# Performance work log

Measured on AMD Instinct MI355X. Metric: run time of the kernel, lower is better.

Reference implementation:

```python
import jax, jax.numpy as jnp
import numpy as np
from jax import lax


def _dense_image_warp(img, flow):
    # TFA semantics: out[b,i,j] = bilinear_sample(img[b], (i - flow[b,i,j,0], j - flow[b,i,j,1]))
    # floors clamped to [0, size-2]; alphas clamped to [0, 1].
    B, H, W, C = img.shape
    gy = jnp.arange(H, dtype=flow.dtype)[None, :, None]
    gx = jnp.arange(W, dtype=flow.dtype)[None, None, :]
    qy = gy - flow[..., 0]
    qx = gx - flow[..., 1]
    fy = jnp.clip(jnp.floor(qy), 0.0, H - 2)
    fx = jnp.clip(jnp.floor(qx), 0.0, W - 2)
    ay = jnp.clip(qy - fy, 0.0, 1.0)[..., None]
    ax = jnp.clip(qx - fx, 0.0, 1.0)[..., None]
    fy = fy.astype(jnp.int32)
    fx = fx.astype(jnp.int32)
    b = jnp.arange(B)[:, None, None]
    tl = img[b, fy, fx]
    tr = img[b, fy, fx + 1]
    bl = img[b, fy + 1, fx]
    br = img[b, fy + 1, fx + 1]
    top = tl + ax * (tr - tl)
    bot = bl + ax * (br - bl)
    return top + ay * (bot - top)


def _conv(x, w, b, act):
    y = lax.conv_general_dilated(x, w, (1, 1), 'SAME',
                                 dimension_numbers=('NHWC', 'HWIO', 'NHWC')) + b
    return jax.nn.relu(y) if act else y


def _predict(x, ws, bs):
    for i in range(4):
        x = _conv(x, ws[i], bs[i], True)
    return _conv(x, ws[4], bs[4], False)  # final 1x1 -> 2 channels, linear


def _upsample2x(x):
    B, H, W, C = x.shape
    return jax.image.resize(x, (B, 2 * H, 2 * W, C), method='bilinear')


# Conv stack dims: in=64 (concat of two 32-ch maps)
_KSHAPES = [(3, 3, 64, 32), (3, 3, 32, 64), (1, 1, 64, 64), (1, 1, 64, 16), (1, 1, 16, 2)]


def setup_inputs() -> dict:
    key = jax.random.key(0)
    ks = jax.random.split(key, 4 + 2 * len(_KSHAPES))
    B, H, W, C = 8, 256, 256, 32
    inp = {
        'input_1': jax.random.normal(ks[0], (B, H, W, C), jnp.float32),
        'input_2': jax.random.normal(ks[1], (B, H, W, C), jnp.float32),
        'flow_1_2': jax.random.normal(ks[2], (B, H, W, 2), jnp.float32) * 3.0,
        'flow_2_1': jax.random.normal(ks[3], (B, H, W, 2), jnp.float32) * 3.0,
    }
    for i, sh in enumerate(_KSHAPES):
        inp[f'w12_{i}'] = jax.random.normal(ks[4 + i], sh, jnp.float32) * 0.05
        inp[f'b12_{i}'] = jnp.zeros((sh[-1],), jnp.float32)
        inp[f'w21_{i}'] = jax.random.normal(ks[4 + len(_KSHAPES) + i], sh, jnp.float32) * 0.05
        inp[f'b21_{i}'] = jnp.zeros((sh[-1],), jnp.float32)
    return inp


def reference(input_1, input_2, flow_1_2, flow_2_1,
              w12_0, b12_0, w12_1, b12_1, w12_2, b12_2, w12_3, b12_3, w12_4, b12_4,
              w21_0, b21_0, w21_1, b21_1, w21_2, b21_2, w21_3, b21_3, w21_4, b21_4):
    ws12 = [w12_0, w12_1, w12_2, w12_3, w12_4]
    bs12 = [b12_0, b12_1, b12_2, b12_3, b12_4]
    ws21 = [w21_0, w21_1, w21_2, w21_3, w21_4]
    bs21 = [b21_0, b21_1, b21_2, b21_3, b21_4]

    # 1 -> 2 direction
    input_1_warped_1 = _dense_image_warp(input_1, flow_1_2)
    flow_change_1_2 = _predict(jnp.concatenate([input_2, input_1_warped_1], axis=3), ws12, bs12)
    flow_1_2_changed = flow_1_2 + flow_change_1_2
    input_1_warped_2 = _dense_image_warp(input_1, flow_1_2_changed)
    flow_1_2_up = _upsample2x(flow_1_2_changed)

    # 2 -> 1 direction
    input_2_warped_1 = _dense_image_warp(input_2, flow_2_1)
    flow_change_2_1 = _predict(jnp.concatenate([input_1, input_2_warped_1], axis=3), ws21, bs21)
    flow_2_1_changed = flow_2_1 + flow_change_2_1
    input_2_warped_2 = _dense_image_warp(input_2, flow_2_1_changed)
    flow_2_1_up = _upsample2x(flow_2_1_changed)

    return (input_1_warped_2, input_2_warped_2, flow_1_2_up, flow_2_1_up)
```

## Files before the change

kernel.cpp:

```cpp
#include <hip/hip_runtime.h>
#include <hip/hip_bf16.h>
#include <cstddef>

#define B_ 8
#define H_ 256
#define W_ 256

static constexpr int NPIX = B_ * H_ * W_;

typedef __attribute__((ext_vector_type(8))) short bf16x8;
typedef __attribute__((ext_vector_type(4))) float f32x4;

__device__ __forceinline__ float4 ld4(const float* p) { return *(const float4*)p; }

__device__ __forceinline__ short f2bf(float x) {
    unsigned u = __float_as_uint(x);
    unsigned r = (u + 0x7fffu + ((u >> 16) & 1u)) >> 16;
    return (short)r;
}

__global__ __launch_bounds__(256) void cvt_inputs_kernel(
    const float* __restrict__ in1, const float* __restrict__ in2,
    short* __restrict__ xb1, short* __restrict__ xb2)
{
    int t = blockIdx.x * 256 + threadIdx.x;
    const int N8 = NPIX * 32 / 8;
    const float* src = (t < N8) ? in1 : in2;
    short* dst = (t < N8) ? xb1 : xb2;
    int i = (t < N8) ? t : t - N8;
    float4 a = ld4(src + (size_t)i * 8);
    float4 b = ld4(src + (size_t)i * 8 + 4);
    bf16x8 r;
    r[0] = f2bf(a.x); r[1] = f2bf(a.y); r[2] = f2bf(a.z); r[3] = f2bf(a.w);
    r[4] = f2bf(b.x); r[5] = f2bf(b.y); r[6] = f2bf(b.z); r[7] = f2bf(b.w);
    *(bf16x8*)(dst + (size_t)i * 8) = r;
}

__global__ __launch_bounds__(256) void prep_weights_kernel(
    const float* __restrict__ w0a, const float* __restrict__ w1a,
    const float* __restrict__ w2a, const float* __restrict__ w3a,
    const float* __restrict__ w0b, const float* __restrict__ w1b,
    const float* __restrict__ w2b, const float* __restrict__ w3b,
    short* __restrict__ wt0, short* __restrict__ wt1)
{
    int t = blockIdx.x * 256 + threadIdx.x;
    if (t >= 2 * 5248) return;
    int dir = t / 5248;
    int r = t % 5248;
    const float* w0 = dir ? w0b : w0a;
    const float* w1 = dir ? w1b : w1a;
    const float* w2 = dir ? w2b : w2a;
    const float* w3 = dir ? w3b : w3a;
    short* wt = dir ? wt1 : wt0;
    bf16x8 v;
    if (r < 2304) {
        int l = r & 63, n = (r >> 6) & 1, c = (r >> 7) & 1, tp = r >> 8;
#pragma unroll
        for (int j = 0; j < 8; ++j) {
            int ci = c * 32 + 8 * (l >> 4) + j;
            int co = n * 16 + (l & 15);
            v[j] = f2bf(w0[(size_t)(tp * 64 + ci) * 32 + co]);
        }
    } else if (r < 4608) {
        int q = r - 2304;
        int l = q & 63, n = (q >> 6) & 3, tp = q >> 8;
#pragma unroll
        for (int j = 0; j < 8; ++j) {
            int ci = 8 * (l >> 4) + j;
            int co = n * 16 + (l & 15);
            v[j] = f2bf(w1[(size_t)(tp * 32 + ci) * 64 + co]);
        }
    } else if (r < 5120) {
        int q = r - 4608;
        int l = q & 63, n = (q >> 6) & 3, c = q >> 8;
#pragma unroll
        for (int j = 0; j < 8; ++j) {
            int k = 32 * c + 8 * (l >> 4) + j;
            int co = n * 16 + (l & 15);
            v[j] = f2bf(w2[(size_t)k * 64 + co]);
        }
    } else {
        int q = r - 5120;
        int l = q & 63, c = q >> 6;
#pragma unroll
        for (int j = 0; j < 8; ++j) {
            int k = 32 * c + 8 * (l >> 4) + j;
            v[j] = f2bf(w3[(size_t)k * 16 + (l & 15)]);
        }
    }
    *(bf16x8*)(wt + (size_t)r * 8) = v;
}

__global__ __launch_bounds__(256) void warp_bf16_kernel(
    const float* __restrict__ img, const float* __restrict__ flow,
    short* __restrict__ out)
{
    int gid = blockIdx.x * 256 + threadIdx.x;
    int p   = gid >> 3;
    int c4  = (gid & 7) << 2;
    int b   = p >> 16;
    int i   = (p >> 8) & 255;
    int j   = p & 255;
    float2 f = *(const float2*)(flow + (size_t)p * 2);
    float qy = (float)i - f.x;
    float qx = (float)j - f.y;
    float fyf = fminf(fmaxf(floorf(qy), 0.0f), (float)(H_ - 2));
    float fxf = fminf(fmaxf(floorf(qx), 0.0f), (float)(W_ - 2));
    float ay = fminf(fmaxf(qy - fyf, 0.0f), 1.0f);
    float ax = fminf(fmaxf(qx - fxf, 0.0f), 1.0f);
    int fy = (int)fyf, fx = (int)fxf;
    const float* base = img + ((((size_t)b * H_ + fy) * W_ + fx) << 5) + c4;
    float4 tl = ld4(base);
    float4 tr = ld4(base + 32);
    float4 bl = ld4(base + W_ * 32);
    float4 br = ld4(base + W_ * 32 + 32);
    short4 r;
    { float t = tl.x + ax * (tr.x - tl.x); float u = bl.x + ax * (br.x - bl.x); r.x = f2bf(t + ay * (u - t)); }
    { float t = tl.y + ax * (tr.y - tl.y); float u = bl.y + ax * (br.y - bl.y); r.y = f2bf(t + ay * (u - t)); }
    { float t = tl.z + ax * (tr.z - tl.z); float u = bl.z + ax * (br.z - bl.z); r.z = f2bf(t + ay * (u - t)); }
    { float t = tl.w + ax * (tr.w - tl.w); float u = bl.w + ax * (br.w - bl.w); r.w = f2bf(t + ay * (u - t)); }
    *(short4*)(out + ((size_t)p << 5) + c4) = r;
}

__global__ __launch_bounds__(256) void warp_f32_kernel(
    const float* __restrict__ img, const float* __restrict__ flow,
    float* __restrict__ out)
{
    int gid = blockIdx.x * 256 + threadIdx.x;
    int p   = gid >> 3;
    int c4  = (gid & 7) << 2;
    int b   = p >> 16;
    int i   = (p >> 8) & 255;
    int j   = p & 255;
    float2 f = *(const float2*)(flow + (size_t)p * 2);
    float qy = (float)i - f.x;
    float qx = (float)j - f.y;
    float fyf = fminf(fmaxf(floorf(qy), 0.0f), (float)(H_ - 2));
    float fxf = fminf(fmaxf(floorf(qx), 0.0f), (float)(W_ - 2));
    float ay = fminf(fmaxf(qy - fyf, 0.0f), 1.0f);
    float ax = fminf(fmaxf(qx - fxf, 0.0f), 1.0f);
    int fy = (int)fyf, fx = (int)fxf;
    const float* base = img + ((((size_t)b * H_ + fy) * W_ + fx) << 5) + c4;
    float4 tl = ld4(base);
    float4 tr = ld4(base + 32);
    float4 bl = ld4(base + W_ * 32);
    float4 br = ld4(base + W_ * 32 + 32);
    float4 r;
    { float t = tl.x + ax * (tr.x - tl.x); float u = bl.x + ax * (br.x - bl.x); r.x = t + ay * (u - t); }
    { float t = tl.y + ax * (tr.y - tl.y); float u = bl.y + ax * (br.y - bl.y); r.y = t + ay * (u - t); }
    { float t = tl.z + ax * (tr.z - tl.z); float u = bl.z + ax * (br.z - bl.z); r.z = t + ay * (u - t); }
    { float t = tl.w + ax * (tr.w - tl.w); float u = bl.w + ax * (br.w - bl.w); r.w = t + ay * (u - t); }
    *(float4*)(out + ((size_t)p << 5) + c4) = r;
}

__global__ __launch_bounds__(512) void conv0_mfma_kernel(
    const short* __restrict__ xA, const short* __restrict__ xB,
    const short* __restrict__ wtab, const float* __restrict__ bias,
    short* __restrict__ h0)
{
    __shared__ short swt[2304 * 8];
    int tid = threadIdx.x;
    for (int i = tid; i < 2304; i += 512)
        ((bf16x8*)swt)[i] = ((const bf16x8*)wtab)[i];
    __syncthreads();

    int wave = tid >> 6, lane = tid & 63;
    int l15 = lane & 15, g = lane >> 4;
    int pbase = blockIdx.x * 128 + wave * 16;
    int px = pbase + l15;
    int y  = (px >> 8) & 255;
    int xl = px & 255;

    const short* ap = xA + ((size_t)px << 5) + g * 8;
    const short* bp = xB + ((size_t)px << 5) + g * 8;
    const bf16x8* wfrag = (const bf16x8*)swt;

    float bv0 = bias[l15], bv1 = bias[16 + l15];
    f32x4 acc0 = {bv0, bv0, bv0, bv0};
    f32x4 acc1 = {bv1, bv1, bv1, bv1};
    const bf16x8 z8 = {0, 0, 0, 0, 0, 0, 0, 0};

#pragma unroll
    for (int dy = -1; dy <= 1; ++dy) {
        if ((unsigned)(y + dy) >= (unsigned)H_) continue;
#pragma unroll
        for (int dx = -1; dx <= 1; ++dx) {
            bool v = (unsigned)(xl + dx) < (unsigned)W_;
            int off = (dy * W_ + (v ? dx : 0)) << 5;
            bf16x8 a0 = *(const bf16x8*)(ap + off);
            bf16x8 a1 = *(const bf16x8*)(bp + off);
            a0 = v ? a0 : z8;
            a1 = v ? a1 : z8;
            int t = (dy + 1) * 3 + (dx + 1);
            acc0 = __builtin_amdgcn_mfma_f32_16x16x32_bf16(a0, wfrag[(t * 4 + 0) * 64 + lane], acc0, 0, 0, 0);
            acc1 = __builtin_amdgcn_mfma_f32_16x16x32_bf16(a0, wfrag[(t * 4 + 1) * 64 + lane], acc1, 0, 0, 0);
            acc0 = __builtin_amdgcn_mfma_f32_16x16x32_bf16(a1, wfrag[(t * 4 + 2) * 64 + lane], acc0, 0, 0, 0);
            acc1 = __builtin_amdgcn_mfma_f32_16x16x32_bf16(a1, wfrag[(t * 4 + 3) * 64 + lane], acc1, 0, 0, 0);
        }
    }

#pragma unroll
    for (int r = 0; r < 4; ++r) {
        size_t row = (size_t)(pbase + g * 4 + r) << 5;
        h0[row + l15]      = f2bf(fmaxf(acc0[r], 0.f));
        h0[row + 16 + l15] = f2bf(fmaxf(acc1[r], 0.f));
    }
}

__global__ __launch_bounds__(512) void conv1_mfma_kernel(
    const short* __restrict__ h0, const short* __restrict__ wtab,
    const float* __restrict__ b1, const float* __restrict__ b2,
    const float* __restrict__ b3, const float* __restrict__ w4,
    const float* __restrict__ b4, const float* __restrict__ flow,
    float* __restrict__ fc)
{
    __shared__ short swt[2944 * 8];
    __shared__ __align__(16) short sx[8][1024];
    int tid = threadIdx.x;
    for (int i = tid; i < 2944; i += 512)
        ((bf16x8*)swt)[i] = ((const bf16x8*)wtab)[i];
    __syncthreads();

    int wave = tid >> 6, lane = tid & 63;
    int l15 = lane & 15, g = lane >> 4;
    int pbase = blockIdx.x * 128 + wave * 16;
    int px = pbase + l15;
    int y  = (px >> 8) & 255;
    int xl = px & 255;

    const short* ap = h0 + ((size_t)px << 5) + g * 8;
    const bf16x8* W1 = (const bf16x8*)swt;
    const bf16x8* W2 = (const bf16x8*)swt + 2304;
    const bf16x8* W3 = (const bf16x8*)swt + 2816;
    char* xb = (char*)&sx[wave][0];
    const bf16x8 z8 = {0, 0, 0, 0, 0, 0, 0, 0};

    f32x4 acc[4];
#pragma unroll
    for (int n = 0; n < 4; ++n) {
        float b = b1[n * 16 + l15];
        acc[n] = (f32x4){b, b, b, b};
    }
#pragma unroll
    for (int dy = -1; dy <= 1; ++dy) {
        if ((unsigned)(y + dy) >= (unsigned)H_) continue;
#pragma unroll
        for (int dx = -1; dx <= 1; ++dx) {
            bool v = (unsigned)(xl + dx) < (unsigned)W_;
            int off = (dy * W_ + (v ? dx : 0)) << 5;
            bf16x8 a = *(const bf16x8*)(ap + off);
            a = v ? a : z8;
            int t = (dy + 1) * 3 + (dx + 1);
#pragma unroll
            for (int n = 0; n < 4; ++n)
                acc[n] = __builtin_amdgcn_mfma_f32_16x16x32_bf16(a, W1[(t * 4 + n) * 64 + lane], acc[n], 0, 0, 0);
        }
    }
#pragma unroll
    for (int n = 0; n < 4; ++n)
#pragma unroll
        for (int r = 0; r < 4; ++r) {
            int row = g * 4 + r, ch = n * 16 + l15;
            int byte = (row * 128 + ch * 2) ^ ((row & 7) << 4);
            *(short*)(xb + byte) = f2bf(fmaxf(acc[n][r], 0.f));
        }

#pragma unroll
    for (int n = 0; n < 4; ++n) {
        float b = b2[n * 16 + l15];
        acc[n] = (f32x4){b, b, b, b};
    }
#pragma unroll
    for (int c = 0; c < 2; ++c) {
        int byte = (l15 * 128 + (32 * c + 8 * g) * 2) ^ ((l15 & 7) << 4);
        bf16x8 a = *(const bf16x8*)(xb + byte);
#pragma unroll
        for (int n = 0; n < 4; ++n)
            acc[n] = __builtin_amdgcn_mfma_f32_16x16x32_bf16(a, W2[(c * 4 + n) * 64 + lane], acc[n], 0, 0, 0);
    }
#pragma unroll
    for (int n = 0; n < 4; ++n)
#pragma unroll
        for (int r = 0; r < 4; ++r) {
            int row = g * 4 + r, ch = n * 16 + l15;
            int byte = (row * 128 + ch * 2) ^ ((row & 7) << 4);
            *(short*)(xb + byte) = f2bf(fmaxf(acc[n][r], 0.f));
        }

    float b3v = b3[l15];
    f32x4 acc3 = {b3v, b3v, b3v, b3v};
#pragma unroll
    for (int c = 0; c < 2; ++c) {
        int byte = (l15 * 128 + (32 * c + 8 * g) * 2) ^ ((l15 & 7) << 4);
        bf16x8 a = *(const bf16x8*)(xb + byte);
        acc3 = __builtin_amdgcn_mfma_f32_16x16x32_bf16(a, W3[c * 64 + lane], acc3, 0, 0, 0);
    }

    float w40 = w4[l15 * 2 + 0], w41 = w4[l15 * 2 + 1];
    float bb0 = b4[0], bb1 = b4[1];
#pragma unroll
    for (int r = 0; r < 4; ++r) {
        float v = fmaxf(acc3[r], 0.f);
        float s0 = v * w40, s1 = v * w41;
#pragma unroll
        for (int m = 1; m < 16; m <<= 1) {
            s0 += __shfl_xor(s0, m);
            s1 += __shfl_xor(s1, m);
        }
        if (l15 == 0) {
            int pr = pbase + g * 4 + r;
            float2 fl = *(const float2*)(flow + (size_t)pr * 2);
            float2 o; o.x = fl.x + bb0 + s0; o.y = fl.y + bb1 + s1;
            *(float2*)(fc + (size_t)pr * 2) = o;
        }
    }
}

__global__ __launch_bounds__(256) void upsample_kernel(
    const float* __restrict__ fc, float* __restrict__ out)
{
    int gid = blockIdx.x * 256 + threadIdx.x;
    int b  = gid >> 18;
    int oy = (gid >> 9) & 511;
    int ox = gid & 511;
    float iy = 0.5f * (float)oy - 0.25f;
    float ix = 0.5f * (float)ox - 0.25f;
    float y0f = floorf(iy), x0f = floorf(ix);
    float wy = iy - y0f, wx = ix - x0f;
    int y0 = min(max((int)y0f, 0), H_ - 1);
    int y1 = min(max((int)y0f + 1, 0), H_ - 1);
    int x0 = min(max((int)x0f, 0), W_ - 1);
    int x1 = min(max((int)x0f + 1, 0), W_ - 1);
    float2 v00 = *(const float2*)(fc + (((size_t)b * H_ + y0) * W_ + x0) * 2);
    float2 v01 = *(const float2*)(fc + (((size_t)b * H_ + y0) * W_ + x1) * 2);
    float2 v10 = *(const float2*)(fc + (((size_t)b * H_ + y1) * W_ + x0) * 2);
    float2 v11 = *(const float2*)(fc + (((size_t)b * H_ + y1) * W_ + x1) * 2);
    float2 r;
    { float t = v00.x + wx * (v01.x - v00.x); float u = v10.x + wx * (v11.x - v10.x); r.x = t + wy * (u - t); }
    { float t = v00.y + wx * (v01.y - v00.y); float u = v10.y + wx * (v11.y - v10.y); r.y = t + wy * (u - t); }
    *(float2*)(out + (size_t)gid * 2) = r;
}

extern "C" void kernel_launch(void* const* d_in, const int* in_sizes, int n_in,
                              void* d_out, int out_size, void* d_ws, size_t ws_size,
                              hipStream_t stream)
{
    (void)in_sizes; (void)n_in; (void)out_size; (void)ws_size;
    const float* input1 = (const float*)d_in[0];
    const float* input2 = (const float*)d_in[1];
    char* wsb = (char*)d_ws;
    short* xb1  = (short*)(wsb);
    short* xb2  = (short*)(wsb + 33554432);
    short* wbf  = (short*)(wsb + 67108864);
    short* h0   = (short*)(wsb + 100663296);
    float* fcbuf= (float*)(wsb + 134217728);
    short* wt0  = (short*)(wsb + 138412032);
    short* wt1  = (short*)(wsb + 138412032 + 5248 * 16);
    float* outf = (float*)d_out;

    cvt_inputs_kernel<<<NPIX * 64 / 8 / 256, 256, 0, stream>>>(input1, input2, xb1, xb2);
    prep_weights_kernel<<<(2 * 5248 + 255) / 256, 256, 0, stream>>>(
        (const float*)d_in[4],  (const float*)d_in[8],  (const float*)d_in[12], (const float*)d_in[16],
        (const float*)d_in[6],  (const float*)d_in[10], (const float*)d_in[14], (const float*)d_in[18],
        wt0, wt1);

    for (int d = 0; d < 2; ++d) {
        const float* src   = (d == 0) ? input1 : input2;
        const short* xoth  = (d == 0) ? xb2 : xb1;
        const float* flow  = (const float*)d_in[2 + d];
        short* wt = (d == 0) ? wt0 : wt1;
        const float* b0 = (const float*)d_in[5 + 2 * d];
        const float* b1 = (const float*)d_in[9 + 2 * d];
        const float* b2 = (const float*)d_in[13 + 2 * d];
        const float* b3 = (const float*)d_in[17 + 2 * d];
        const float* w4 = (const float*)d_in[20 + 2 * d];
        const float* b4 = (const float*)d_in[21 + 2 * d];
        float* out_warp = outf + (size_t)d * NPIX * 32;
        float* out_up   = outf + (size_t)2 * NPIX * 32 + (size_t)d * (B_ * 512 * 512 * 2);

        warp_bf16_kernel<<<NPIX * 8 / 256, 256, 0, stream>>>(src, flow, wbf);
        conv0_mfma_kernel<<<NPIX / 128, 512, 0, stream>>>(xoth, wbf, wt, b0, h0);
        conv1_mfma_kernel<<<NPIX / 128, 512, 0, stream>>>(h0, wt + 2304 * 8, b1, b2, b3, w4, b4, flow, fcbuf);
        warp_f32_kernel<<<NPIX * 8 / 256, 256, 0, stream>>>(src, fcbuf, out_warp);
        upsample_kernel<<<B_ * 512 * 512 / 256, 256, 0, stream>>>(fcbuf, out_up);
    }
}
```

Before: 616.1 us.

## Batch both flow directions per launch and double pixels per wave in convs

The two direction passes are merged into single launches of each kernel, indexed by a direction bit, with the workspace buffers doubled so both directions stay live at once. The conv kernels now give each wave 32 pixels (two MFMA row tiles) instead of 16, so every weight fragment read from shared memory feeds two MFMAs. Each block covers a full image row and loads its weights once for twice as many pixels. This cuts launch count and weight-load overhead and gives larger grids, at the cost of more registers, doubled LDS scratch per wave and a larger workspace footprint.

```diff
diff --git a/kernel.cpp b/kernel.cpp
--- a/kernel.cpp
+++ b/kernel.cpp
@@ -92,12 +92,19 @@
 }
 
 __global__ __launch_bounds__(256) void warp_bf16_kernel(
-    const float* __restrict__ img, const float* __restrict__ flow,
-    short* __restrict__ out)
+    const float* __restrict__ in1, const float* __restrict__ in2,
+    const float* __restrict__ fl12, const float* __restrict__ fl21,
+    short* __restrict__ wbf)
 {
     int gid = blockIdx.x * 256 + threadIdx.x;
-    int p   = gid >> 3;
-    int c4  = (gid & 7) << 2;
+    int d   = (gid >= NPIX * 8);
+    int g2  = gid - (d ? NPIX * 8 : 0);
+    const float* img  = d ? in2 : in1;
+    const float* flow = d ? fl21 : fl12;
+    short* out = wbf + (size_t)d * NPIX * 32;
+
+    int p   = g2 >> 3;
+    int c4  = (g2 & 7) << 2;
     int b   = p >> 16;
     int i   = (p >> 8) & 255;
     int j   = p & 255;
@@ -123,12 +130,18 @@
 }
 
 __global__ __launch_bounds__(256) void warp_f32_kernel(
-    const float* __restrict__ img, const float* __restrict__ flow,
-    float* __restrict__ out)
+    const float* __restrict__ in1, const float* __restrict__ in2,
+    const float* __restrict__ fcb, float* __restrict__ outf)
 {
     int gid = blockIdx.x * 256 + threadIdx.x;
-    int p   = gid >> 3;
-    int c4  = (gid & 7) << 2;
+    int d   = (gid >= NPIX * 8);
+    int g2  = gid - (d ? NPIX * 8 : 0);
+    const float* img  = d ? in2 : in1;
+    const float* flow = fcb + (size_t)d * NPIX * 2;
+    float* out = outf + (size_t)d * NPIX * 32;
+
+    int p   = g2 >> 3;
+    int c4  = (g2 & 7) << 2;
     int b   = p >> 16;
     int i   = (p >> 8) & 255;
     int j   = p & 255;
@@ -154,11 +167,21 @@
 }
 
 __global__ __launch_bounds__(512) void conv0_mfma_kernel(
-    const short* __restrict__ xA, const short* __restrict__ xB,
-    const short* __restrict__ wtab, const float* __restrict__ bias,
+    const short* __restrict__ xb1, const short* __restrict__ xb2,
+    const short* __restrict__ wbf,
+    const short* __restrict__ wt0, const short* __restrict__ wt1,
+    const float* __restrict__ b0a, const float* __restrict__ b0b,
     short* __restrict__ h0)
 {
     __shared__ short swt[2304 * 8];
+    int d   = blockIdx.x >> 11;
+    int bid = blockIdx.x & 2047;
+    const short* xoth = d ? xb1 : xb2;
+    const short* xw   = wbf + (size_t)d * NPIX * 32;
+    const short* wtab = d ? wt1 : wt0;
+    const float* bias = d ? b0b : b0a;
+    short* out = h0 + (size_t)d * NPIX * 32;
+
     int tid = threadIdx.x;
     for (int i = tid; i < 2304; i += 512)
         ((bf16x8*)swt)[i] = ((const bf16x8*)wtab)[i];
@@ -166,18 +189,23 @@
 
     int wave = tid >> 6, lane = tid & 63;
     int l15 = lane & 15, g = lane >> 4;
-    int pbase = blockIdx.x * 128 + wave * 16;
-    int px = pbase + l15;
-    int y  = (px >> 8) & 255;
-    int xl = px & 255;
-
-    const short* ap = xA + ((size_t)px << 5) + g * 8;
-    const short* bp = xB + ((size_t)px << 5) + g * 8;
+    int prow = bid * 256;
+    int y    = bid & 255;
+    int t0   = prow + wave * 32;
+    int xl0  = wave * 32 + l15;
+    int xl1  = xl0 + 16;
+
+    const short* a0p = xoth + ((size_t)(t0 + l15) << 5) + g * 8;
+    const short* a1p = a0p + (16 << 5);
+    const short* b0p = xw + ((size_t)(t0 + l15) << 5) + g * 8;
+    const short* b1p = b0p + (16 << 5);
     const bf16x8* wfrag = (const bf16x8*)swt;
 
     float bv0 = bias[l15], bv1 = bias[16 + l15];
-    f32x4 acc0 = {bv0, bv0, bv0, bv0};
-    f32x4 acc1 = {bv1, bv1, bv1, bv1};
+    f32x4 acc00 = {bv0, bv0, bv0, bv0};
+    f32x4 acc01 = {bv1, bv1, bv1, bv1};
+    f32x4 acc10 = {bv0, bv0, bv0, bv0};
+    f32x4 acc11 = {bv1, bv1, bv1, bv1};
     const bf16x8 z8 = {0, 0, 0, 0, 0, 0, 0, 0};
 
 #pragma unroll
@@ -185,37 +213,68 @@
         if ((unsigned)(y + dy) >= (unsigned)H_) continue;
 #pragma unroll
         for (int dx = -1; dx <= 1; ++dx) {
-            bool v = (unsigned)(xl + dx) < (unsigned)W_;
-            int off = (dy * W_ + (v ? dx : 0)) << 5;
-            bf16x8 a0 = *(const bf16x8*)(ap + off);
-            bf16x8 a1 = *(const bf16x8*)(bp + off);
-            a0 = v ? a0 : z8;
-            a1 = v ? a1 : z8;
+            bool v0 = (unsigned)(xl0 + dx) < (unsigned)W_;
+            bool v1 = (unsigned)(xl1 + dx) < (unsigned)W_;
+            int off0 = (dy * W_ + (v0 ? dx : 0)) << 5;
+            int off1 = (dy * W_ + (v1 ? dx : 0)) << 5;
+            bf16x8 aA0 = *(const bf16x8*)(a0p + off0);
+            bf16x8 aB0 = *(const bf16x8*)(b0p + off0);
+            bf16x8 aA1 = *(const bf16x8*)(a1p + off1);
+            bf16x8 aB1 = *(const bf16x8*)(b1p + off1);
+            aA0 = v0 ? aA0 : z8;  aB0 = v0 ? aB0 : z8;
+            aA1 = v1 ? aA1 : z8;  aB1 = v1 ? aB1 : z8;
             int t = (dy + 1) * 3 + (dx + 1);
-            acc0 = __builtin_amdgcn_mfma_f32_16x16x32_bf16(a0, wfrag[(t * 4 + 0) * 64 + lane], acc0, 0, 0, 0);
-            acc1 = __builtin_amdgcn_mfma_f32_16x16x32_bf16(a0, wfrag[(t * 4 + 1) * 64 + lane], acc1, 0, 0, 0);
-            acc0 = __builtin_amdgcn_mfma_f32_16x16x32_bf16(a1, wfrag[(t * 4 + 2) * 64 + lane], acc0, 0, 0, 0);
-            acc1 = __builtin_amdgcn_mfma_f32_16x16x32_bf16(a1, wfrag[(t * 4 + 3) * 64 + lane], acc1, 0, 0, 0);
+            bf16x8 w0 = wfrag[(t * 4 + 0) * 64 + lane];
+            bf16x8 w1 = wfrag[(t * 4 + 1) * 64 + lane];
+            bf16x8 w2 = wfrag[(t * 4 + 2) * 64 + lane];
+            bf16x8 w3 = wfrag[(t * 4 + 3) * 64 + lane];
+            acc00 = __builtin_amdgcn_mfma_f32_16x16x32_bf16(aA0, w0, acc00, 0, 0, 0);
+            acc01 = __builtin_amdgcn_mfma_f32_16x16x32_bf16(aA0, w1, acc01, 0, 0, 0);
+            acc10 = __builtin_amdgcn_mfma_f32_16x16x32_bf16(aA1, w0, acc10, 0, 0, 0);
+            acc11 = __builtin_amdgcn_mfma_f32_16x16x32_bf16(aA1, w1, acc11, 0, 0, 0);
+            acc00 = __builtin_amdgcn_mfma_f32_16x16x32_bf16(aB0, w2, acc00, 0, 0, 0);
+            acc01 = __builtin_amdgcn_mfma_f32_16x16x32_bf16(aB0, w3, acc01, 0, 0, 0);
+            acc10 = __builtin_amdgcn_mfma_f32_16x16x32_bf16(aB1, w2, acc10, 0, 0, 0);
+            acc11 = __builtin_amdgcn_mfma_f32_16x16x32_bf16(aB1, w3, acc11, 0, 0, 0);
         }
     }
 
 #pragma unroll
     for (int r = 0; r < 4; ++r) {
-        size_t row = (size_t)(pbase + g * 4 + r) << 5;
-        h0[row + l15]      = f2bf(fmaxf(acc0[r], 0.f));
-        h0[row + 16 + l15] = f2bf(fmaxf(acc1[r], 0.f));
+        size_t r0 = (size_t)(t0 + g * 4 + r) << 5;
+        size_t r1 = (size_t)(t0 + 16 + g * 4 + r) << 5;
+        out[r0 + l15]      = f2bf(fmaxf(acc00[r], 0.f));
+        out[r0 + 16 + l15] = f2bf(fmaxf(acc01[r], 0.f));
+        out[r1 + l15]      = f2bf(fmaxf(acc10[r], 0.f));
+        out[r1 + 16 + l15] = f2bf(fmaxf(acc11[r], 0.f));
     }
 }
 
 __global__ __launch_bounds__(512) void conv1_mfma_kernel(
-    const short* __restrict__ h0, const short* __restrict__ wtab,
-    const float* __restrict__ b1, const float* __restrict__ b2,
-    const float* __restrict__ b3, const float* __restrict__ w4,
-    const float* __restrict__ b4, const float* __restrict__ flow,
-    float* __restrict__ fc)
+    const short* __restrict__ h0,
+    const short* __restrict__ wt0, const short* __restrict__ wt1,
+    const float* __restrict__ b1a, const float* __restrict__ b1b,
+    const float* __restrict__ b2a, const float* __restrict__ b2b,
+    const float* __restrict__ b3a, const float* __restrict__ b3b,
+    const float* __restrict__ w4a, const float* __restrict__ w4b,
+    const float* __restrict__ b4a, const float* __restrict__ b4b,
+    const float* __restrict__ fl12, const float* __restrict__ fl21,
+    float* __restrict__ fcb)
 {
     __shared__ short swt[2944 * 8];
-    __shared__ __align__(16) short sx[8][1024];
+    __shared__ __align__(16) short sx[8][2048];
+    int d   = blockIdx.x >> 11;
+    int bid = blockIdx.x & 2047;
+    const short* hsrc = h0 + (size_t)d * NPIX * 32;
+    const short* wtab = (d ? wt1 : wt0) + 2304 * 8;
+    const float* b1 = d ? b1b : b1a;
+    const float* b2 = d ? b2b : b2a;
+    const float* b3 = d ? b3b : b3a;
+    const float* w4 = d ? w4b : w4a;
+    const float* b4 = d ? b4b : b4a;
+    const float* flow = d ? fl21 : fl12;
+    float* fc = fcb + (size_t)d * NPIX * 2;
+
     int tid = threadIdx.x;
     for (int i = tid; i < 2944; i += 512)
         ((bf16x8*)swt)[i] = ((const bf16x8*)wtab)[i];
@@ -223,106 +282,141 @@
 
     int wave = tid >> 6, lane = tid & 63;
     int l15 = lane & 15, g = lane >> 4;
-    int pbase = blockIdx.x * 128 + wave * 16;
-    int px = pbase + l15;
-    int y  = (px >> 8) & 255;
-    int xl = px & 255;
-
-    const short* ap = h0 + ((size_t)px << 5) + g * 8;
+    int prow = bid * 256;
+    int y    = bid & 255;
+    int t0   = prow + wave * 32;
+    int xl0  = wave * 32 + l15;
+    int xl1  = xl0 + 16;
+
+    const short* a0p = hsrc + ((size_t)(t0 + l15) << 5) + g * 8;
+    const short* a1p = a0p + (16 << 5);
     const bf16x8* W1 = (const bf16x8*)swt;
     const bf16x8* W2 = (const bf16x8*)swt + 2304;
     const bf16x8* W3 = (const bf16x8*)swt + 2816;
     char* xb = (char*)&sx[wave][0];
     const bf16x8 z8 = {0, 0, 0, 0, 0, 0, 0, 0};
 
-    f32x4 acc[4];
+    f32x4 acc0[4], acc1[4];
 #pragma unroll
     for (int n = 0; n < 4; ++n) {
         float b = b1[n * 16 + l15];
-        acc[n] = (f32x4){b, b, b, b};
+        acc0[n] = (f32x4){b, b, b, b};
+        acc1[n] = (f32x4){b, b, b, b};
     }
 #pragma unroll
     for (int dy = -1; dy <= 1; ++dy) {
         if ((unsigned)(y + dy) >= (unsigned)H_) continue;
 #pragma unroll
         for (int dx = -1; dx <= 1; ++dx) {
-            bool v = (unsigned)(xl + dx) < (unsigned)W_;
-            int off = (dy * W_ + (v ? dx : 0)) << 5;
-            bf16x8 a = *(const bf16x8*)(ap + off);
-            a = v ? a : z8;
+            bool v0 = (unsigned)(xl0 + dx) < (unsigned)W_;
+            bool v1 = (unsigned)(xl1 + dx) < (unsigned)W_;
+            int off0 = (dy * W_ + (v0 ? dx : 0)) << 5;
+            int off1 = (dy * W_ + (v1 ? dx : 0)) << 5;
+            bf16x8 a0 = *(const bf16x8*)(a0p + off0);
+            bf16x8 a1 = *(const bf16x8*)(a1p + off1);
+            a0 = v0 ? a0 : z8;
+            a1 = v1 ? a1 : z8;
             int t = (dy + 1) * 3 + (dx + 1);
 #pragma unroll
-            for (int n = 0; n < 4; ++n)
-                acc[n] = __builtin_amdgcn_mfma_f32_16x16x32_bf16(a, W1[(t * 4 + n) * 64 + lane], acc[n], 0, 0, 0);
+            for (int n = 0; n < 4; ++n) {
+                bf16x8 w = W1[(t * 4 + n) * 64 + lane];
+                acc0[n] = __builtin_amdgcn_mfma_f32_16x16x32_bf16(a0, w, acc0[n], 0, 0, 0);
+                acc1[n] = __builtin_amdgcn_mfma_f32_16x16x32_bf16(a1, w, acc1[n], 0, 0, 0);
+            }
         }
     }
 #pragma unroll
     for (int n = 0; n < 4; ++n)
 #pragma unroll
         for (int r = 0; r < 4; ++r) {
-            int row = g * 4 + r, ch = n * 16 + l15;
-            int byte = (row * 128 + ch * 2) ^ ((row & 7) << 4);
-            *(short*)(xb + byte) = f2bf(fmaxf(acc[n][r], 0.f));
+            int row0 = g * 4 + r, ch = n * 16 + l15;
+            int by0 = (row0 * 128 + ch * 2) ^ ((row0 & 7) << 4);
+            int by1 = ((row0 + 16) * 128 + ch * 2) ^ ((row0 & 7) << 4);
+            *(short*)(xb + by0) = f2bf(fmaxf(acc0[n][r], 0.f));
+            *(short*)(xb + by1) = f2bf(fmaxf(acc1[n][r], 0.f));
         }
 
 #pragma unroll
     for (int n = 0; n < 4; ++n) {
         float b = b2[n * 16 + l15];
-        acc[n] = (f32x4){b, b, b, b};
+        acc0[n] = (f32x4){b, b, b, b};
+        acc1[n] = (f32x4){b, b, b, b};
     }
 #pragma unroll
     for (int c = 0; c < 2; ++c) {
-        int byte = (l15 * 128 + (32 * c + 8 * g) * 2) ^ ((l15 & 7) << 4);
-        bf16x8 a = *(const bf16x8*)(xb + byte);
-#pragma unroll
-        for (int n = 0; n < 4; ++n)
-            acc[n] = __builtin_amdgcn_mfma_f32_16x16x32_bf16(a, W2[(c * 4 + n) * 64 + lane], acc[n], 0, 0, 0);
+        int by0 = (l15 * 128 + (32 * c + 8 * g) * 2) ^ ((l15 & 7) << 4);
+        int by1 = ((l15 + 16) * 128 + (32 * c + 8 * g) * 2) ^ ((l15 & 7) << 4);
+        bf16x8 a0 = *(const bf16x8*)(xb + by0);
+        bf16x8 a1 = *(const bf16x8*)(xb + by1);
+#pragma unroll
+        for (int n = 0; n < 4; ++n) {
+            bf16x8 w = W2[(c * 4 + n) * 64 + lane];
+            acc0[n] = __builtin_amdgcn_mfma_f32_16x16x32_bf16(a0, w, acc0[n], 0, 0, 0);
+            acc1[n] = __builtin_amdgcn_mfma_f32_16x16x32_bf16(a1, w, acc1[n], 0, 0, 0);
+        }
     }
 #pragma unroll
     for (int n = 0; n < 4; ++n)
 #pragma unroll
         for (int r = 0; r < 4; ++r) {
-            int row = g * 4 + r, ch = n * 16 + l15;
-            int byte = (row * 128 + ch * 2) ^ ((row & 7) << 4);
-            *(short*)(xb + byte) = f2bf(fmaxf(acc[n][r], 0.f));
+            int row0 = g * 4 + r, ch = n * 16 + l15;
+            int by0 = (row0 * 128 + ch * 2) ^ ((row0 & 7) << 4);
+            int by1 = ((row0 + 16) * 128 + ch * 2) ^ ((row0 & 7) << 4);
+            *(short*)(xb + by0) = f2bf(fmaxf(acc0[n][r], 0.f));
+            *(short*)(xb + by1) = f2bf(fmaxf(acc1[n][r], 0.f));
         }
 
     float b3v = b3[l15];
-    f32x4 acc3 = {b3v, b3v, b3v, b3v};
+    f32x4 acc3a = {b3v, b3v, b3v, b3v};
+    f32x4 acc3b = {b3v, b3v, b3v, b3v};
 #pragma unroll
     for (int c = 0; c < 2; ++c) {
-        int byte = (l15 * 128 + (32 * c + 8 * g) * 2) ^ ((l15 & 7) << 4);
-        bf16x8 a = *(const bf16x8*)(xb + byte);
-        acc3 = __builtin_amdgcn_mfma_f32_16x16x32_bf16(a, W3[c * 64 + lane], acc3, 0, 0, 0);
+        int by0 = (l15 * 128 + (32 * c + 8 * g) * 2) ^ ((l15 & 7) << 4);
+        int by1 = ((l15 + 16) * 128 + (32 * c + 8 * g) * 2) ^ ((l15 & 7) << 4);
+        bf16x8 a0 = *(const bf16x8*)(xb + by0);
+        bf16x8 a1 = *(const bf16x8*)(xb + by1);
+        bf16x8 w = W3[c * 64 + lane];
+        acc3a = __builtin_amdgcn_mfma_f32_16x16x32_bf16(a0, w, acc3a, 0, 0, 0);
+        acc3b = __builtin_amdgcn_mfma_f32_16x16x32_bf16(a1, w, acc3b, 0, 0, 0);
     }
 
     float w40 = w4[l15 * 2 + 0], w41 = w4[l15 * 2 + 1];
     float bb0 = b4[0], bb1 = b4[1];
 #pragma unroll
-    for (int r = 0; r < 4; ++r) {
-        float v = fmaxf(acc3[r], 0.f);
-        float s0 = v * w40, s1 = v * w41;
-#pragma unroll
-        for (int m = 1; m < 16; m <<= 1) {
-            s0 += __shfl_xor(s0, m);
-            s1 += __shfl_xor(s1, m);
-        }
-        if (l15 == 0) {
-            int pr = pbase + g * 4 + r;
-            float2 fl = *(const float2*)(flow + (size_t)pr * 2);
-            float2 o; o.x = fl.x + bb0 + s0; o.y = fl.y + bb1 + s1;
-            *(float2*)(fc + (size_t)pr * 2) = o;
+    for (int tt = 0; tt < 2; ++tt) {
+        f32x4 a3 = tt ? acc3b : acc3a;
+#pragma unroll
+        for (int r = 0; r < 4; ++r) {
+            float v = fmaxf(a3[r], 0.f);
+            float s0 = v * w40, s1 = v * w41;
+#pragma unroll
+            for (int m = 1; m < 16; m <<= 1) {
+                s0 += __shfl_xor(s0, m);
+                s1 += __shfl_xor(s1, m);
+            }
+            if (l15 == 0) {
+                int pr = t0 + tt * 16 + g * 4 + r;
+                float2 fl = *(const float2*)(flow + (size_t)pr * 2);
+                float2 o; o.x = fl.x + bb0 + s0; o.y = fl.y + bb1 + s1;
+                *(float2*)(fc + (size_t)pr * 2) = o;
+            }
         }
     }
 }
 
 __global__ __launch_bounds__(256) void upsample_kernel(
-    const float* __restrict__ fc, float* __restrict__ out)
+    const float* __restrict__ fcb, float* __restrict__ outup)
 {
     int gid = blockIdx.x * 256 + threadIdx.x;
-    int b  = gid >> 18;
-    int oy = (gid >> 9) & 511;
-    int ox = gid & 511;
+    const int NUP = B_ * 512 * 512;
+    int d  = (gid >= NUP);
+    int g2 = gid - (d ? NUP : 0);
+    const float* fc = fcb + (size_t)d * NPIX * 2;
+    float* out = outup + (size_t)d * NUP * 2;
+
+    int b  = g2 >> 18;
+    int oy = (g2 >> 9) & 511;
+    int ox = g2 & 511;
     float iy = 0.5f * (float)oy - 0.25f;
     float ix = 0.5f * (float)ox - 0.25f;
     float y0f = floorf(iy), x0f = floorf(ix);
@@ -338,7 +432,7 @@
     float2 r;
     { float t = v00.x + wx * (v01.x - v00.x); float u = v10.x + wx * (v11.x - v10.x); r.x = t + wy * (u - t); }
     { float t = v00.y + wx * (v01.y - v00.y); float u = v10.y + wx * (v11.y - v10.y); r.y = t + wy * (u - t); }
-    *(float2*)(out + (size_t)gid * 2) = r;
+    *(float2*)(out + (size_t)g2 * 2) = r;
 }
 
 extern "C" void kernel_launch(void* const* d_in, const int* in_sizes, int n_in,
@@ -348,40 +442,36 @@
     (void)in_sizes; (void)n_in; (void)out_size; (void)ws_size;
     const float* input1 = (const float*)d_in[0];
     const float* input2 = (const float*)d_in[1];
+    const float* fl12 = (const float*)d_in[2];
+    const float* fl21 = (const float*)d_in[3];
     char* wsb = (char*)d_ws;
     short* xb1  = (short*)(wsb);
     short* xb2  = (short*)(wsb + 33554432);
     short* wbf  = (short*)(wsb + 67108864);
-    short* h0   = (short*)(wsb + 100663296);
-    float* fcbuf= (float*)(wsb + 134217728);
-    short* wt0  = (short*)(wsb + 138412032);
-    short* wt1  = (short*)(wsb + 138412032 + 5248 * 16);
+    short* h0   = (short*)(wsb + 134217728);
+    float* fcb  = (float*)(wsb + 201326592);
+    short* wt0  = (short*)(wsb + 209715200);
+    short* wt1  = (short*)(wsb + 209715200 + 5248 * 16);
     float* outf = (float*)d_out;
+    float* outup = outf + (size_t)2 * NPIX * 32;
 
     cvt_inputs_kernel<<<NPIX * 64 / 8 / 256, 256, 0, stream>>>(input1, input2, xb1, xb2);
     prep_weights_kernel<<<(2 * 5248 + 255) / 256, 256, 0, stream>>>(
         (const float*)d_in[4],  (const float*)d_in[8],  (const float*)d_in[12], (const float*)d_in[16],
         (const float*)d_in[6],  (const float*)d_in[10], (const float*)d_in[14], (const float*)d_in[18],
         wt0, wt1);
-
-    for (int d = 0; d < 2; ++d) {
-        const float* src   = (d == 0) ? input1 : input2;
-        const short* xoth  = (d == 0) ? xb2 : xb1;
-        const float* flow  = (const float*)d_in[2 + d];
-        short* wt = (d == 0) ? wt0 : wt1;
-        const float* b0 = (const float*)d_in[5 + 2 * d];
-        const float* b1 = (const float*)d_in[9 + 2 * d];
-        const float* b2 = (const float*)d_in[13 + 2 * d];
-        const float* b3 = (const float*)d_in[17 + 2 * d];
-        const float* w4 = (const float*)d_in[20 + 2 * d];
-        const float* b4 = (const float*)d_in[21 + 2 * d];
-        float* out_warp = outf + (size_t)d * NPIX * 32;
-        float* out_up   = outf + (size_t)2 * NPIX * 32 + (size_t)d * (B_ * 512 * 512 * 2);
-
-        warp_bf16_kernel<<<NPIX * 8 / 256, 256, 0, stream>>>(src, flow, wbf);
-        conv0_mfma_kernel<<<NPIX / 128, 512, 0, stream>>>(xoth, wbf, wt, b0, h0);
-        conv1_mfma_kernel<<<NPIX / 128, 512, 0, stream>>>(h0, wt + 2304 * 8, b1, b2, b3, w4, b4, flow, fcbuf);
-        warp_f32_kernel<<<NPIX * 8 / 256, 256, 0, stream>>>(src, fcbuf, out_warp);
-        upsample_kernel<<<B_ * 512 * 512 / 256, 256, 0, stream>>>(fcbuf, out_up);
-    }
-}
+    warp_bf16_kernel<<<2 * NPIX * 8 / 256, 256, 0, stream>>>(input1, input2, fl12, fl21, wbf);
+    conv0_mfma_kernel<<<2 * NPIX / 256, 512, 0, stream>>>(
+        xb1, xb2, wbf, wt0, wt1,
+        (const float*)d_in[5], (const float*)d_in[7], h0);
+    conv1_mfma_kernel<<<2 * NPIX / 256, 512, 0, stream>>>(
+        h0, wt0, wt1,
+        (const float*)d_in[9],  (const float*)d_in[11],
+        (const float*)d_in[13], (const float*)d_in[15],
+        (const float*)d_in[17], (const float*)d_in[19],
+        (const float*)d_in[20], (const float*)d_in[22],
+        (const float*)d_in[21], (const float*)d_in[23],
+        fl12, fl21, fcb);
+    warp_f32_kernel<<<2 * NPIX * 8 / 256, 256, 0, stream>>>(input1, input2, fcb, outf);
+    upsample_kernel<<<2 * B_ * 512 * 512 / 256, 256, 0, stream>>>(fcb, outup);
+}
```

Measured after the change: 593.2 us. 1.04x faster.
